# Optimization experiments

Hardware: AMD Instinct MI355X
Metric: run time of the kernel (lower is better)

The kernel has to match this reference:

```python
import jax, jax.numpy as jnp
import numpy as np

DIM = 768
HEADS = 12
HEAD_DIM = DIM // HEADS
SCALE = HEAD_DIM ** -0.5
EPS = 1e-6


def setup_inputs() -> dict:
    key = jax.random.key(0)
    ks = jax.random.split(key, 10)
    B, Nq, Nk, C = 4, 4096, 4096, DIM
    std = C ** -0.5
    return {
        "x_q": jax.random.normal(ks[0], (B, Nq, C), jnp.float32),
        "x_kv": jax.random.normal(ks[1], (B, Nk, C), jnp.float32),
        "Wq": jax.random.normal(ks[2], (C, C), jnp.float32) * std,
        "bq": jnp.zeros((C,), jnp.float32),
        "Wk": jax.random.normal(ks[3], (C, C), jnp.float32) * std,
        "bk": jnp.zeros((C,), jnp.float32),
        "Wv": jax.random.normal(ks[4], (C, C), jnp.float32) * std,
        "bv": jnp.zeros((C,), jnp.float32),
        "Wp": jax.random.normal(ks[5], (C, C), jnp.float32) * std,
        "bp": jnp.zeros((C,), jnp.float32),
    }


def _phi(x):
    # ELU(alpha=1) + 1 positive feature map
    return jax.nn.elu(x) + 1.0


def reference(x_q, x_kv, Wq, bq, Wk, bk, Wv, bv, Wp, bp):
    B, Nq, C = x_q.shape
    Nk = x_kv.shape[1]
    h, d = HEADS, HEAD_DIM
    # projections (torch Linear: x @ W.T + b)
    q = x_q @ Wq.T + bq   # [B,Nq,C]
    k = x_kv @ Wk.T + bk  # [B,Nk,C]
    v = x_kv @ Wv.T + bv  # [B,Nk,C]
    # split heads -> [B,h,N,d]
    q = q.reshape(B, Nq, h, d).transpose(0, 2, 1, 3) * SCALE
    k = k.reshape(B, Nk, h, d).transpose(0, 2, 1, 3)
    v = v.reshape(B, Nk, h, d).transpose(0, 2, 1, 3)
    q_phi = _phi(q)
    k_phi = _phi(k)
    # KV state [B,h,d,d] and normalizer sum [B,h,d]
    kv = jnp.einsum('bhnd,bhne->bhde', k_phi, v)
    k_sum = k_phi.sum(axis=2)
    out = jnp.einsum('bhnd,bhde->bhne', q_phi, kv)
    z = jnp.einsum('bhnd,bhd->bhn', q_phi, k_sum)[..., None] + EPS
    out = out / z
    out = out.transpose(0, 2, 1, 3).reshape(B, Nq, C)
    return out @ Wp.T + bp
```

## Files before the change

### kernel.cpp

```cpp
#include <hip/hip_runtime.h>
#include <hip/hip_bf16.h>
#include <cstdint>
#include <cstddef>

#define HD_B   4
#define SEQ    4096
#define CDIM   768
#define HEADS  12
#define HDIM   64
#define MROWS  (HD_B * SEQ)
#define QSCALE 0.125f
#define EPSV   1e-6f

typedef __attribute__((ext_vector_type(8))) short  short8v;
typedef __attribute__((ext_vector_type(4))) float  f32x4;

__device__ __forceinline__ unsigned short f2b(float f) {
    unsigned int u = __float_as_uint(f);
    u += 0x7FFFu + ((u >> 16) & 1u);
    return (unsigned short)(u >> 16);
}
__device__ __forceinline__ float b2f(unsigned short b) {
    return __uint_as_float(((unsigned int)b) << 16);
}
__device__ __forceinline__ float phi_f(float x) {
    return x > 0.f ? x + 1.f : __expf(x);
}

#define GLOAD_LDS16(g, l)                                             \
    __builtin_amdgcn_global_load_lds(                                 \
        (__attribute__((address_space(1))) void*)(void*)(g),          \
        (__attribute__((address_space(3))) void*)(l), 16, 0, 0)

#define VMW12() asm volatile("s_waitcnt vmcnt(12)" ::: "memory")
#define VMW8()  asm volatile("s_waitcnt vmcnt(8)"  ::: "memory")
#define VMW4()  asm volatile("s_waitcnt vmcnt(4)"  ::: "memory")
#define VMW0()  asm volatile("s_waitcnt vmcnt(0)"  ::: "memory")
#define LGW()   asm volatile("s_waitcnt lgkmcnt(0)" ::: "memory")
#define SB()    do { __builtin_amdgcn_sched_barrier(0);               \
                     __builtin_amdgcn_s_barrier();                    \
                     __builtin_amdgcn_sched_barrier(0); } while (0)

__global__ void wcvt_all(const float* __restrict__ wq, const float* __restrict__ wk,
                         const float* __restrict__ wv, const float* __restrict__ wp,
                         unsigned short* __restrict__ dst) {
    const int y = blockIdx.y;
    const float* src = (y == 0) ? wq : (y == 1) ? wk : (y == 2) ? wv : wp;
    const int i = blockIdx.x * 256 + threadIdx.x;
    float4 v = reinterpret_cast<const float4*>(src)[i];
    ushort4 o;
    o.x = f2b(v.x); o.y = f2b(v.y); o.z = f2b(v.z); o.w = f2b(v.w);
    reinterpret_cast<ushort4*>(dst + (size_t)y * (CDIM * CDIM))[i] = o;
}

template <int KIND>
__global__ __launch_bounds__(256) void gemm_cnt(
    const float* __restrict__ Aq,
    const float* __restrict__ Akv,
    const unsigned short* __restrict__ Abf,
    const unsigned short* __restrict__ Wb,
    const float* __restrict__ b0, const float* __restrict__ b1,
    const float* __restrict__ b2,
    unsigned short* __restrict__ out_q, unsigned short* __restrict__ out_k,
    unsigned short* __restrict__ out_v, float* __restrict__ out_f)
{
    constexpr int K  = CDIM;
    constexpr int NC = (KIND == 0) ? 18 : 6;
    constexpr int T  = NC * 128;
    constexpr int NT = K / 64;

    __shared__ __align__(16) char smem[65536];

    const int tid  = threadIdx.x;
    const int lane = tid & 63;
    const int w    = tid >> 6;
    const int wr   = w >> 1, wc = w & 1;

    const int bid  = blockIdx.x;
    const int s    = (bid & 7) * (T >> 3) + (bid >> 3);
    const int colp = s % NC;
    const int rowp = s / NC;
    const int brow = rowp * 128;
    const int mode = (KIND == 0) ? (colp / 6) : 3;
    const int bcol = (KIND == 0) ? (colp % 6) * 128 : colp * 128;

    const float* A32          = (KIND == 0) ? (mode == 0 ? Aq : Akv) : nullptr;
    const unsigned short* Bp  = Wb + ((KIND == 0) ? (size_t)mode * (K * K) : 0);

    const int r8  = lane >> 3;
    const int c8e = ((lane & 7) ^ r8) << 3;
    const int ar  = lane >> 4;
    const int ac  = (lane & 15) << 2;
    const int fr  = lane & 15;
    const int hi4 = lane >> 4;

    f32x4 acc[4][4];
#pragma unroll
    for (int i = 0; i < 4; ++i)
#pragma unroll
        for (int j = 0; j < 4; ++j)
            acc[i][j] = (f32x4){0.f, 0.f, 0.f, 0.f};

    auto stageB = [&](int buf, int kt) {
        char* dst = smem + 32768 + buf * 16384;
#pragma unroll
        for (int g = 0; g < 4; ++g) {
            const unsigned short* src =
                Bp + (size_t)(bcol + w * 32 + g * 8 + r8) * K + kt * 64 + c8e;
            GLOAD_LDS16(src, dst + (w * 32 + g * 8) * 128);
        }
    };
    auto stageA16 = [&](int buf, int kt) {
        char* dst = smem + buf * 16384;
#pragma unroll
        for (int g = 0; g < 4; ++g) {
            const unsigned short* src =
                Abf + (size_t)(brow + w * 32 + g * 8 + r8) * K + kt * 64 + c8e;
            GLOAD_LDS16(src, dst + (w * 32 + g * 8) * 128);
        }
    };
    float4 fA[8];
    auto aload = [&](int kt) {
#pragma unroll
        for (int j = 0; j < 8; ++j)
            fA[j] = *(const float4*)(A32 + (size_t)(brow + w * 32 + j * 4 + ar) * K
                                     + kt * 64 + ac);
    };
    auto awrite = [&](int buf) {
        char* dst = smem + buf * 16384;
#pragma unroll
        for (int j = 0; j < 8; ++j) {
            const int row = w * 32 + j * 4 + ar;
            unsigned int p0, p1;
            asm("v_cvt_pk_bf16_f32 %0, %1, %2" : "=v"(p0) : "v"(fA[j].x), "v"(fA[j].y));
            asm("v_cvt_pk_bf16_f32 %0, %1, %2" : "=v"(p1) : "v"(fA[j].z), "v"(fA[j].w));
            uint2 pk; pk.x = p0; pk.y = p1;
            *(uint2*)(dst + row * 128 + ((ac << 1) ^ ((row & 7) << 4))) = pk;
        }
    };
    auto compute = [&](int buf) {
        const char* Ab = smem + buf * 16384;
        const char* Bb = smem + 32768 + buf * 16384;
        short8v a[4][2];
#pragma unroll
        for (int i = 0; i < 4; ++i) {
            const int row = wr * 64 + i * 16 + fr;
#pragma unroll
            for (int ks = 0; ks < 2; ++ks)
                a[i][ks] = *(const short8v*)(Ab + row * 128 +
                              ((((ks << 2) + hi4) ^ (row & 7)) << 4));
        }
#pragma unroll
        for (int j = 0; j < 4; ++j) {
            const int row = wc * 64 + j * 16 + fr;
            short8v bb0 = *(const short8v*)(Bb + row * 128 + ((hi4 ^ (row & 7)) << 4));
            short8v bb1 = *(const short8v*)(Bb + row * 128 + (((4 + hi4) ^ (row & 7)) << 4));
#pragma unroll
            for (int i = 0; i < 4; ++i) {
                acc[i][j] = __builtin_amdgcn_mfma_f32_16x16x32_bf16(a[i][0], bb0, acc[i][j], 0, 0, 0);
                acc[i][j] = __builtin_amdgcn_mfma_f32_16x16x32_bf16(a[i][1], bb1, acc[i][j], 0, 0, 0);
            }
        }
    };

    if (KIND == 0) {
        aload(0);
        stageB(0, 0);
        VMW4();
        awrite(0);
        aload(1);
        stageB(1, 1);
        LGW();
        SB();
        for (int t = 0; t < NT; ++t) {
            const int c = t & 1;
            if (t == NT - 1) { VMW0(); } else { VMW12(); }
            SB();
            compute(c);
            SB();
            if (t < NT - 1) {
                VMW4();
                awrite(c ^ 1);
                if (t < NT - 2) { aload(t + 2); stageB(c, t + 2); }
                LGW();
            }
        }
    } else {
        stageA16(0, 0); stageB(0, 0);
        stageA16(1, 1); stageB(1, 1);
        for (int t = 0; t < NT; ++t) {
            const int c = t & 1;
            if (t == NT - 1) { VMW0(); } else { VMW8(); }
            SB();
            compute(c);
            SB();
            if (t < NT - 2) { stageA16(c, t + 2); stageB(c, t + 2); }
        }
    }

    float* ep = (float*)(void*)smem + w * (16 * 68);
    const int rr = lane >> 2;
    const int cb = (lane & 3) * 4;
    const float* bptr = (KIND == 1) ? b0 : (mode == 0 ? b0 : (mode == 1 ? b1 : b2));
    unsigned short* o16 = (KIND == 0)
        ? (mode == 0 ? out_q : (mode == 1 ? out_k : out_v)) : nullptr;

    float4 bb[4];
#pragma unroll
    for (int q = 0; q < 4; ++q)
        bb[q] = *(const float4*)&bptr[bcol + wc * 64 + q * 16 + cb];

#pragma unroll
    for (int i = 0; i < 4; ++i) {
#pragma unroll
        for (int j = 0; j < 4; ++j)
#pragma unroll
            for (int r = 0; r < 4; ++r)
                ep[(hi4 * 4 + r) * 68 + j * 16 + fr] = acc[i][j][r];
#pragma unroll
        for (int q = 0; q < 4; ++q) {
            const int cc = q * 16 + cb;
            f32x4 v = *(const f32x4*)&ep[rr * 68 + cc];
            const int rg = brow + wr * 64 + i * 16 + rr;
            const int cg = bcol + wc * 64 + cc;
            const float4 bq = bb[q];
            if (KIND == 1) {
                float4 ov;
                ov.x = v[0] + bq.x; ov.y = v[1] + bq.y;
                ov.z = v[2] + bq.z; ov.w = v[3] + bq.w;
                *(float4*)(out_f + (size_t)rg * 768 + cg) = ov;
            } else {
                ushort4 ov;
                if (mode == 0) {
                    ov.x = f2b(phi_f((v[0] + bq.x) * QSCALE));
                    ov.y = f2b(phi_f((v[1] + bq.y) * QSCALE));
                    ov.z = f2b(phi_f((v[2] + bq.z) * QSCALE));
                    ov.w = f2b(phi_f((v[3] + bq.w) * QSCALE));
                } else if (mode == 1) {
                    ov.x = f2b(phi_f(v[0] + bq.x));
                    ov.y = f2b(phi_f(v[1] + bq.y));
                    ov.z = f2b(phi_f(v[2] + bq.z));
                    ov.w = f2b(phi_f(v[3] + bq.w));
                } else {
                    ov.x = f2b(v[0] + bq.x);
                    ov.y = f2b(v[1] + bq.y);
                    ov.z = f2b(v[2] + bq.z);
                    ov.w = f2b(v[3] + bq.w);
                }
                *(ushort4*)(o16 + (size_t)rg * 768 + cg) = ov;
            }
        }
    }
}

#define KVCH   128
#define KVITER 2
#define NCHUNK 16

__global__ __launch_bounds__(256) void kv_part(
    const unsigned short* __restrict__ kphi,
    const unsigned short* __restrict__ vmat,
    float* __restrict__ part)
{
    const int bh = blockIdx.y;
    const int b  = bh / HEADS, h = bh % HEADS;
    const int c  = blockIdx.x;
    __shared__ float Kl[KVCH][HDIM];
    __shared__ float Vl[KVCH][HDIM];
    const int t  = threadIdx.x;
    const int i  = t >> 2;
    const int jb = t & 3;

    float acc[16];
#pragma unroll
    for (int jj = 0; jj < 16; ++jj) acc[jj] = 0.f;
    float ksum = 0.f;

    for (int it = 0; it < KVITER; ++it) {
        const size_t rbase = (size_t)b * SEQ + (size_t)c * (KVCH * KVITER) + it * KVCH;
        __syncthreads();
        for (int l = 0; l < KVCH / 32; ++l) {
            int row = l * 32 + (t >> 3);
            int col = (t & 7) << 3;
            const size_t g = (rbase + row) * CDIM + h * HDIM + col;
            int4 kk = *(const int4*)(kphi + g);
            int4 vv = *(const int4*)(vmat + g);
            const unsigned short* kp = (const unsigned short*)&kk;
            const unsigned short* vp = (const unsigned short*)&vv;
#pragma unroll
            for (int q = 0; q < 8; ++q) {
                Kl[row][col + q] = b2f(kp[q]);
                Vl[row][col + q] = b2f(vp[q]);
            }
        }
        __syncthreads();
        for (int n = 0; n < KVCH; ++n) {
            float kf = Kl[n][i];
            const float4* vr = (const float4*)&Vl[n][jb * 16];
            float4 v0 = vr[0], v1 = vr[1], v2 = vr[2], v3 = vr[3];
            acc[0]  += kf * v0.x; acc[1]  += kf * v0.y; acc[2]  += kf * v0.z; acc[3]  += kf * v0.w;
            acc[4]  += kf * v1.x; acc[5]  += kf * v1.y; acc[6]  += kf * v1.z; acc[7]  += kf * v1.w;
            acc[8]  += kf * v2.x; acc[9]  += kf * v2.y; acc[10] += kf * v2.z; acc[11] += kf * v2.w;
            acc[12] += kf * v3.x; acc[13] += kf * v3.y; acc[14] += kf * v3.z; acc[15] += kf * v3.w;
            ksum += kf;
        }
    }
    float* op = part + ((size_t)c * 48 + bh) * 4160;
#pragma unroll
    for (int jj = 0; jj < 16; ++jj) op[i * 64 + jb * 16 + jj] = acc[jj];
    if (jb == 0) op[4096 + i] = ksum;
}

__global__ void kv_finalize(const float* __restrict__ part, float* __restrict__ kv) {
    int idx = blockIdx.x * 256 + threadIdx.x;
    if (idx >= 48 * 4160) return;
    float s = 0.f;
    for (int c = 0; c < NCHUNK; ++c) s += part[(size_t)c * 48 * 4160 + idx];
    kv[idx] = s;
}

__global__ __launch_bounds__(256) void attn_apply(
    const unsigned short* __restrict__ qphi,
    const float* __restrict__ kv,
    unsigned short* __restrict__ attn)
{
    const int h  = blockIdx.y;
    const int m0 = blockIdx.x * 64;
    const int b  = m0 >> 12;
    const int bh = b * HEADS + h;
    __shared__ float kvs[HDIM][HDIM];
    __shared__ float ksums[HDIM];
    __shared__ unsigned short ql[64][HDIM];
    const int t = threadIdx.x;
    const float* kvp = kv + (size_t)bh * 4160;
#pragma unroll
    for (int it = 0; it < 4; ++it) {
        int e = it * 1024 + t * 4;
        *(float4*)&kvs[e >> 6][e & 63] = *(const float4*)&kvp[e];
    }
    if (t < 64) ksums[t] = kvp[4096 + t];
#pragma unroll
    for (int it = 0; it < 2; ++it) {
        int row = it * 32 + (t >> 3);
        int col = (t & 7) << 3;
        *(int4*)&ql[row][col] =
            *(const int4*)(qphi + (size_t)(m0 + row) * CDIM + h * HDIM + col);
    }
    __syncthreads();

    const int r  = t >> 2;
    const int jb = t & 3;
    float acc[16];
#pragma unroll
    for (int jj = 0; jj < 16; ++jj) acc[jj] = 0.f;
    float z = 0.f;
    for (int q8 = 0; q8 < 8; ++q8) {
        short8v qv = *(const short8v*)&ql[r][q8 * 8];
#pragma unroll
        for (int dd = 0; dd < 8; ++dd) {
            float qd = b2f((unsigned short)qv[dd]);
            int d = q8 * 8 + dd;
            const float4* kr = (const float4*)&kvs[d][jb * 16];
            float4 k0 = kr[0], k1 = kr[1], k2 = kr[2], k3 = kr[3];
            acc[0]  += qd * k0.x; acc[1]  += qd * k0.y; acc[2]  += qd * k0.z; acc[3]  += qd * k0.w;
            acc[4]  += qd * k1.x; acc[5]  += qd * k1.y; acc[6]  += qd * k1.z; acc[7]  += qd * k1.w;
            acc[8]  += qd * k2.x; acc[9]  += qd * k2.y; acc[10] += qd * k2.z; acc[11] += qd * k2.w;
            acc[12] += qd * k3.x; acc[13] += qd * k3.y; acc[14] += qd * k3.z; acc[15] += qd * k3.w;
            z += qd * ksums[d];
        }
    }
    const float inv = 1.f / (z + EPSV);
    unsigned short* op = attn + (size_t)(m0 + r) * CDIM + h * HDIM + jb * 16;
#pragma unroll
    for (int jj = 0; jj < 16; ++jj) op[jj] = f2b(acc[jj] * inv);
}

extern "C" void kernel_launch(void* const* d_in, const int* in_sizes, int n_in,
                              void* d_out, int out_size, void* d_ws, size_t ws_size,
                              hipStream_t stream)
{
    const float* x_q  = (const float*)d_in[0];
    const float* x_kv = (const float*)d_in[1];
    const float* Wq   = (const float*)d_in[2];
    const float* bq   = (const float*)d_in[3];
    const float* Wk   = (const float*)d_in[4];
    const float* bk   = (const float*)d_in[5];
    const float* Wv   = (const float*)d_in[6];
    const float* bv   = (const float*)d_in[7];
    const float* Wp   = (const float*)d_in[8];
    const float* bp   = (const float*)d_in[9];
    float* out = (float*)d_out;

    char* ws = (char*)d_ws;
    size_t off = 0;
    auto alloc = [&](size_t bytes) -> char* {
        char* p = ws + off;
        off += (bytes + 255) & ~(size_t)255;
        return p;
    };
    const size_t xelems = (size_t)MROWS * CDIM;
    const size_t welems = (size_t)CDIM * CDIM;

    unsigned short* w16    = (unsigned short*)alloc(4 * welems * 2);
    unsigned short* wp16   = w16 + 3 * welems;
    unsigned short* qphi   = (unsigned short*)alloc(xelems * 2);
    unsigned short* kphi   = (unsigned short*)alloc(xelems * 2);
    unsigned short* v16    = (unsigned short*)alloc(xelems * 2);
    unsigned short* attn16 = (unsigned short*)alloc(xelems * 2);
    float* part = (float*)alloc((size_t)NCHUNK * 48 * 4160 * 4);
    float* kvf  = (float*)alloc((size_t)48 * 4160 * 4);

    wcvt_all<<<dim3(576, 4), 256, 0, stream>>>(Wq, Wk, Wv, Wp, w16);

    gemm_cnt<0><<<2304, 256, 0, stream>>>(
        x_q, x_kv, nullptr, w16, bq, bk, bv, qphi, kphi, v16, nullptr);

    kv_part<<<dim3(NCHUNK, 48), 256, 0, stream>>>(kphi, v16, part);
    kv_finalize<<<(48 * 4160 + 255) / 256, 256, 0, stream>>>(part, kvf);
    attn_apply<<<dim3(MROWS / 64, HEADS), 256, 0, stream>>>(qphi, kvf, attn16);

    gemm_cnt<1><<<768, 256, 0, stream>>>(
        nullptr, nullptr, attn16, wp16, bp, nullptr, nullptr,
        nullptr, nullptr, nullptr, out);
}
```

Before: 223.0 us.

## Split Q projection into simple GEMM and single-buffer A tiles in KV/proj GEMMs

Replaces the fused QKV GEMM with a standalone single-buffered Q-projection kernel and a combined K/V GEMM that treats Wk and Wv as one contiguous 1536-row weight. The K/V and output-projection GEMMs now keep only a single LDS buffer for A (register-staged) with a double-buffered B, cutting shared memory from 64KB to 48KB and adding launch_bounds(256,3) to raise occupancy. The output-projection A tile moves from direct global-to-LDS loads to register staging. The cost is less latency hiding in the unpipelined Q kernel and an extra kernel launch.

```diff
diff --git a/kernel.cpp b/kernel.cpp
--- a/kernel.cpp
+++ b/kernel.cpp
@@ -53,39 +53,23 @@
     reinterpret_cast<ushort4*>(dst + (size_t)y * (CDIM * CDIM))[i] = o;
 }
 
-template <int KIND>
-__global__ __launch_bounds__(256) void gemm_cnt(
-    const float* __restrict__ Aq,
-    const float* __restrict__ Akv,
-    const unsigned short* __restrict__ Abf,
-    const unsigned short* __restrict__ Wb,
-    const float* __restrict__ b0, const float* __restrict__ b1,
-    const float* __restrict__ b2,
-    unsigned short* __restrict__ out_q, unsigned short* __restrict__ out_k,
-    unsigned short* __restrict__ out_v, float* __restrict__ out_f)
+__global__ __launch_bounds__(256) void gemm_q(
+    const float* __restrict__ A32,
+    const unsigned short* __restrict__ Bp,
+    const float* __restrict__ bias,
+    unsigned short* __restrict__ outp)
 {
-    constexpr int K  = CDIM;
-    constexpr int NC = (KIND == 0) ? 18 : 6;
-    constexpr int T  = NC * 128;
-    constexpr int NT = K / 64;
-
-    __shared__ __align__(16) char smem[65536];
+    constexpr int K = CDIM;
+    __shared__ __align__(16) char smem[32768];
+    char* As = smem;
+    char* Bs = smem + 16384;
 
     const int tid  = threadIdx.x;
     const int lane = tid & 63;
     const int w    = tid >> 6;
     const int wr   = w >> 1, wc = w & 1;
-
-    const int bid  = blockIdx.x;
-    const int s    = (bid & 7) * (T >> 3) + (bid >> 3);
-    const int colp = s % NC;
-    const int rowp = s / NC;
-    const int brow = rowp * 128;
-    const int mode = (KIND == 0) ? (colp / 6) : 3;
-    const int bcol = (KIND == 0) ? (colp % 6) * 128 : colp * 128;
-
-    const float* A32          = (KIND == 0) ? (mode == 0 ? Aq : Akv) : nullptr;
-    const unsigned short* Bp  = Wb + ((KIND == 0) ? (size_t)mode * (K * K) : 0);
+    const int brow = blockIdx.x * 128;
+    const int bcol = blockIdx.y * 128;
 
     const int r8  = lane >> 3;
     const int c8e = ((lane & 7) ^ r8) << 3;
@@ -101,115 +85,59 @@
         for (int j = 0; j < 4; ++j)
             acc[i][j] = (f32x4){0.f, 0.f, 0.f, 0.f};
 
-    auto stageB = [&](int buf, int kt) {
-        char* dst = smem + 32768 + buf * 16384;
+    for (int k0 = 0; k0 < K; k0 += 64) {
 #pragma unroll
         for (int g = 0; g < 4; ++g) {
             const unsigned short* src =
-                Bp + (size_t)(bcol + w * 32 + g * 8 + r8) * K + kt * 64 + c8e;
-            GLOAD_LDS16(src, dst + (w * 32 + g * 8) * 128);
-        }
-    };
-    auto stageA16 = [&](int buf, int kt) {
-        char* dst = smem + buf * 16384;
-#pragma unroll
-        for (int g = 0; g < 4; ++g) {
-            const unsigned short* src =
-                Abf + (size_t)(brow + w * 32 + g * 8 + r8) * K + kt * 64 + c8e;
-            GLOAD_LDS16(src, dst + (w * 32 + g * 8) * 128);
-        }
-    };
-    float4 fA[8];
-    auto aload = [&](int kt) {
-#pragma unroll
-        for (int j = 0; j < 8; ++j)
-            fA[j] = *(const float4*)(A32 + (size_t)(brow + w * 32 + j * 4 + ar) * K
-                                     + kt * 64 + ac);
-    };
-    auto awrite = [&](int buf) {
-        char* dst = smem + buf * 16384;
+                Bp + (size_t)(bcol + w * 32 + g * 8 + r8) * K + k0 + c8e;
+            GLOAD_LDS16(src, Bs + (w * 32 + g * 8) * 128);
+        }
 #pragma unroll
         for (int j = 0; j < 8; ++j) {
             const int row = w * 32 + j * 4 + ar;
+            float4 f = *(const float4*)(A32 + (size_t)(brow + row) * K + k0 + ac);
             unsigned int p0, p1;
-            asm("v_cvt_pk_bf16_f32 %0, %1, %2" : "=v"(p0) : "v"(fA[j].x), "v"(fA[j].y));
-            asm("v_cvt_pk_bf16_f32 %0, %1, %2" : "=v"(p1) : "v"(fA[j].z), "v"(fA[j].w));
+            asm("v_cvt_pk_bf16_f32 %0, %1, %2" : "=v"(p0) : "v"(f.x), "v"(f.y));
+            asm("v_cvt_pk_bf16_f32 %0, %1, %2" : "=v"(p1) : "v"(f.z), "v"(f.w));
             uint2 pk; pk.x = p0; pk.y = p1;
-            *(uint2*)(dst + row * 128 + ((ac << 1) ^ ((row & 7) << 4))) = pk;
-        }
-    };
-    auto compute = [&](int buf) {
-        const char* Ab = smem + buf * 16384;
-        const char* Bb = smem + 32768 + buf * 16384;
-        short8v a[4][2];
+            *(uint2*)(As + row * 128 + ((ac << 1) ^ ((row & 7) << 4))) = pk;
+        }
+        __syncthreads();
+
+        short8v a[4][2], b[4][2];
 #pragma unroll
         for (int i = 0; i < 4; ++i) {
             const int row = wr * 64 + i * 16 + fr;
 #pragma unroll
             for (int ks = 0; ks < 2; ++ks)
-                a[i][ks] = *(const short8v*)(Ab + row * 128 +
+                a[i][ks] = *(const short8v*)(As + row * 128 +
                               ((((ks << 2) + hi4) ^ (row & 7)) << 4));
         }
 #pragma unroll
         for (int j = 0; j < 4; ++j) {
             const int row = wc * 64 + j * 16 + fr;
-            short8v bb0 = *(const short8v*)(Bb + row * 128 + ((hi4 ^ (row & 7)) << 4));
-            short8v bb1 = *(const short8v*)(Bb + row * 128 + (((4 + hi4) ^ (row & 7)) << 4));
-#pragma unroll
-            for (int i = 0; i < 4; ++i) {
-                acc[i][j] = __builtin_amdgcn_mfma_f32_16x16x32_bf16(a[i][0], bb0, acc[i][j], 0, 0, 0);
-                acc[i][j] = __builtin_amdgcn_mfma_f32_16x16x32_bf16(a[i][1], bb1, acc[i][j], 0, 0, 0);
+#pragma unroll
+            for (int ks = 0; ks < 2; ++ks)
+                b[j][ks] = *(const short8v*)(Bs + row * 128 +
+                              ((((ks << 2) + hi4) ^ (row & 7)) << 4));
+        }
+#pragma unroll
+        for (int i = 0; i < 4; ++i)
+#pragma unroll
+            for (int j = 0; j < 4; ++j) {
+                acc[i][j] = __builtin_amdgcn_mfma_f32_16x16x32_bf16(a[i][0], b[j][0], acc[i][j], 0, 0, 0);
+                acc[i][j] = __builtin_amdgcn_mfma_f32_16x16x32_bf16(a[i][1], b[j][1], acc[i][j], 0, 0, 0);
             }
-        }
-    };
-
-    if (KIND == 0) {
-        aload(0);
-        stageB(0, 0);
-        VMW4();
-        awrite(0);
-        aload(1);
-        stageB(1, 1);
-        LGW();
-        SB();
-        for (int t = 0; t < NT; ++t) {
-            const int c = t & 1;
-            if (t == NT - 1) { VMW0(); } else { VMW12(); }
-            SB();
-            compute(c);
-            SB();
-            if (t < NT - 1) {
-                VMW4();
-                awrite(c ^ 1);
-                if (t < NT - 2) { aload(t + 2); stageB(c, t + 2); }
-                LGW();
-            }
-        }
-    } else {
-        stageA16(0, 0); stageB(0, 0);
-        stageA16(1, 1); stageB(1, 1);
-        for (int t = 0; t < NT; ++t) {
-            const int c = t & 1;
-            if (t == NT - 1) { VMW0(); } else { VMW8(); }
-            SB();
-            compute(c);
-            SB();
-            if (t < NT - 2) { stageA16(c, t + 2); stageB(c, t + 2); }
-        }
+        __syncthreads();
     }
 
     float* ep = (float*)(void*)smem + w * (16 * 68);
     const int rr = lane >> 2;
     const int cb = (lane & 3) * 4;
-    const float* bptr = (KIND == 1) ? b0 : (mode == 0 ? b0 : (mode == 1 ? b1 : b2));
-    unsigned short* o16 = (KIND == 0)
-        ? (mode == 0 ? out_q : (mode == 1 ? out_k : out_v)) : nullptr;
-
     float4 bb[4];
 #pragma unroll
     for (int q = 0; q < 4; ++q)
-        bb[q] = *(const float4*)&bptr[bcol + wc * 64 + q * 16 + cb];
-
+        bb[q] = *(const float4*)&bias[bcol + wc * 64 + q * 16 + cb];
 #pragma unroll
     for (int i = 0; i < 4; ++i) {
 #pragma unroll
@@ -224,19 +152,188 @@
             const int rg = brow + wr * 64 + i * 16 + rr;
             const int cg = bcol + wc * 64 + cc;
             const float4 bq = bb[q];
+            ushort4 ov;
+            ov.x = f2b(phi_f((v[0] + bq.x) * QSCALE));
+            ov.y = f2b(phi_f((v[1] + bq.y) * QSCALE));
+            ov.z = f2b(phi_f((v[2] + bq.z) * QSCALE));
+            ov.w = f2b(phi_f((v[3] + bq.w) * QSCALE));
+            *(ushort4*)(outp + (size_t)rg * 768 + cg) = ov;
+        }
+    }
+}
+
+template <int KIND>
+__global__ __launch_bounds__(256, 3) void gemm_p2(
+    const float* __restrict__ A32,
+    const unsigned short* __restrict__ Abf,
+    const unsigned short* __restrict__ Bp,
+    const float* __restrict__ b0, const float* __restrict__ b1,
+    unsigned short* __restrict__ out_k, unsigned short* __restrict__ out_v,
+    float* __restrict__ out_f)
+{
+    constexpr int K  = CDIM;
+    constexpr int NC = (KIND == 0) ? 12 : 6;
+    constexpr int T  = NC * 128;
+    constexpr int NT = K / 64;
+
+    __shared__ __align__(16) char smem[49152];
+    char* As = smem;
+
+    const int tid  = threadIdx.x;
+    const int lane = tid & 63;
+    const int w    = tid >> 6;
+    const int wr   = w >> 1, wc = w & 1;
+
+    const int bid  = blockIdx.x;
+    const int s    = (bid & 7) * (T >> 3) + (bid >> 3);
+    const int colp = s % NC;
+    const int rowp = s / NC;
+    const int brow = rowp * 128;
+    const int bcol = colp * 128;
+
+    const int r8  = lane >> 3;
+    const int c8e = ((lane & 7) ^ r8) << 3;
+    const int ar  = lane >> 4;
+    const int ac  = (lane & 15) << 2;
+    const int fr  = lane & 15;
+    const int hi4 = lane >> 4;
+
+    f32x4 acc[4][4];
+#pragma unroll
+    for (int i = 0; i < 4; ++i)
+#pragma unroll
+        for (int j = 0; j < 4; ++j)
+            acc[i][j] = (f32x4){0.f, 0.f, 0.f, 0.f};
+
+    auto stageB = [&](int buf, int kt) {
+        char* dst = smem + 16384 + buf * 16384;
+#pragma unroll
+        for (int g = 0; g < 4; ++g) {
+            const unsigned short* src =
+                Bp + (size_t)(bcol + w * 32 + g * 8 + r8) * K + kt * 64 + c8e;
+            GLOAD_LDS16(src, dst + (w * 32 + g * 8) * 128);
+        }
+    };
+
+    float4 fA[8];
+    int4   rAb[4];
+    auto aload = [&](int kt) {
+        if (KIND == 0) {
+#pragma unroll
+            for (int j = 0; j < 8; ++j)
+                fA[j] = *(const float4*)(A32 + (size_t)(brow + w * 32 + j * 4 + ar) * K
+                                         + kt * 64 + ac);
+        } else {
+#pragma unroll
+            for (int g = 0; g < 4; ++g)
+                rAb[g] = *(const int4*)(Abf + (size_t)(brow + w * 32 + g * 8 + r8) * K
+                                        + kt * 64 + ((lane & 7) << 3));
+        }
+    };
+    auto awrite = [&]() {
+        if (KIND == 0) {
+#pragma unroll
+            for (int j = 0; j < 8; ++j) {
+                const int row = w * 32 + j * 4 + ar;
+                unsigned int p0, p1;
+                asm("v_cvt_pk_bf16_f32 %0, %1, %2" : "=v"(p0) : "v"(fA[j].x), "v"(fA[j].y));
+                asm("v_cvt_pk_bf16_f32 %0, %1, %2" : "=v"(p1) : "v"(fA[j].z), "v"(fA[j].w));
+                uint2 pk; pk.x = p0; pk.y = p1;
+                *(uint2*)(As + row * 128 + ((ac << 1) ^ ((row & 7) << 4))) = pk;
+            }
+        } else {
+#pragma unroll
+            for (int g = 0; g < 4; ++g) {
+                const int row = w * 32 + g * 8 + r8;
+                *(int4*)(As + row * 128 + (((lane & 7) ^ r8) << 4)) = rAb[g];
+            }
+        }
+    };
+    auto compute = [&](int bbuf) {
+        const char* Bb = smem + 16384 + bbuf * 16384;
+        short8v a[4][2];
+#pragma unroll
+        for (int i = 0; i < 4; ++i) {
+            const int row = wr * 64 + i * 16 + fr;
+#pragma unroll
+            for (int ks = 0; ks < 2; ++ks)
+                a[i][ks] = *(const short8v*)(As + row * 128 +
+                              ((((ks << 2) + hi4) ^ (row & 7)) << 4));
+        }
+#pragma unroll
+        for (int j = 0; j < 4; ++j) {
+            const int row = wc * 64 + j * 16 + fr;
+            short8v bb0 = *(const short8v*)(Bb + row * 128 + ((hi4 ^ (row & 7)) << 4));
+            short8v bb1 = *(const short8v*)(Bb + row * 128 + (((4 + hi4) ^ (row & 7)) << 4));
+#pragma unroll
+            for (int i = 0; i < 4; ++i) {
+                acc[i][j] = __builtin_amdgcn_mfma_f32_16x16x32_bf16(a[i][0], bb0, acc[i][j], 0, 0, 0);
+                acc[i][j] = __builtin_amdgcn_mfma_f32_16x16x32_bf16(a[i][1], bb1, acc[i][j], 0, 0, 0);
+            }
+        }
+    };
+
+    aload(0);
+    stageB(0, 0);
+    VMW4();
+    awrite();
+    aload(1);
+    stageB(1, 1);
+    LGW();
+    SB();
+
+    for (int t = 0; t < NT; ++t) {
+        const int c = t & 1;
+        if (t == NT - 1) { VMW0(); }
+        else if (KIND == 0) { VMW12(); }
+        else { VMW8(); }
+        SB();
+        compute(c);
+        SB();
+        if (t < NT - 1) {
+            VMW4();
+            awrite();
+            if (t < NT - 2) { aload(t + 2); stageB(c, t + 2); }
+            LGW();
+        }
+    }
+
+    float* ep = (float*)(void*)smem + w * (16 * 68);
+    const int rr = lane >> 2;
+    const int cb = (lane & 3) * 4;
+    const bool isV = (KIND == 0) && (colp >= 6);
+    const float* bptr = (KIND == 1) ? b0 : (isV ? (b1 + (bcol - 768)) : (b0 + bcol));
+    const int colbase = ((KIND == 0 && isV) ? bcol - 768 : bcol) + wc * 64;
+    unsigned short* o16 = isV ? out_v : out_k;
+
+    float4 bb[4];
+#pragma unroll
+    for (int q = 0; q < 4; ++q)
+        bb[q] = (KIND == 1)
+            ? *(const float4*)&bptr[bcol + wc * 64 + q * 16 + cb]
+            : *(const float4*)&bptr[wc * 64 + q * 16 + cb];
+
+#pragma unroll
+    for (int i = 0; i < 4; ++i) {
+#pragma unroll
+        for (int j = 0; j < 4; ++j)
+#pragma unroll
+            for (int r = 0; r < 4; ++r)
+                ep[(hi4 * 4 + r) * 68 + j * 16 + fr] = acc[i][j][r];
+#pragma unroll
+        for (int q = 0; q < 4; ++q) {
+            const int cc = q * 16 + cb;
+            f32x4 v = *(const f32x4*)&ep[rr * 68 + cc];
+            const int rg = brow + wr * 64 + i * 16 + rr;
+            const float4 bq = bb[q];
             if (KIND == 1) {
                 float4 ov;
                 ov.x = v[0] + bq.x; ov.y = v[1] + bq.y;
                 ov.z = v[2] + bq.z; ov.w = v[3] + bq.w;
-                *(float4*)(out_f + (size_t)rg * 768 + cg) = ov;
+                *(float4*)(out_f + (size_t)rg * 768 + (bcol + wc * 64 + cc)) = ov;
             } else {
                 ushort4 ov;
-                if (mode == 0) {
-                    ov.x = f2b(phi_f((v[0] + bq.x) * QSCALE));
-                    ov.y = f2b(phi_f((v[1] + bq.y) * QSCALE));
-                    ov.z = f2b(phi_f((v[2] + bq.z) * QSCALE));
-                    ov.w = f2b(phi_f((v[3] + bq.w) * QSCALE));
-                } else if (mode == 1) {
+                if (!isV) {
                     ov.x = f2b(phi_f(v[0] + bq.x));
                     ov.y = f2b(phi_f(v[1] + bq.y));
                     ov.z = f2b(phi_f(v[2] + bq.z));
@@ -247,7 +344,7 @@
                     ov.z = f2b(v[2] + bq.z);
                     ov.w = f2b(v[3] + bq.w);
                 }
-                *(ushort4*)(o16 + (size_t)rg * 768 + cg) = ov;
+                *(ushort4*)(o16 + (size_t)rg * 768 + (colbase + cc)) = ov;
             }
         }
     }
@@ -402,6 +499,7 @@
     const size_t welems = (size_t)CDIM * CDIM;
 
     unsigned short* w16    = (unsigned short*)alloc(4 * welems * 2);
+    unsigned short* wkv16  = w16 + welems;
     unsigned short* wp16   = w16 + 3 * welems;
     unsigned short* qphi   = (unsigned short*)alloc(xelems * 2);
     unsigned short* kphi   = (unsigned short*)alloc(xelems * 2);
@@ -412,14 +510,15 @@
 
     wcvt_all<<<dim3(576, 4), 256, 0, stream>>>(Wq, Wk, Wv, Wp, w16);
 
-    gemm_cnt<0><<<2304, 256, 0, stream>>>(
-        x_q, x_kv, nullptr, w16, bq, bk, bv, qphi, kphi, v16, nullptr);
+    gemm_q<<<dim3(128, 6), 256, 0, stream>>>(x_q, w16, bq, qphi);
+
+    gemm_p2<0><<<1536, 256, 0, stream>>>(
+        x_kv, nullptr, wkv16, bk, bv, kphi, v16, nullptr);
 
     kv_part<<<dim3(NCHUNK, 48), 256, 0, stream>>>(kphi, v16, part);
     kv_finalize<<<(48 * 4160 + 255) / 256, 256, 0, stream>>>(part, kvf);
     attn_apply<<<dim3(MROWS / 64, HEADS), 256, 0, stream>>>(qphi, kvf, attn16);
 
-    gemm_cnt<1><<<768, 256, 0, stream>>>(
-        nullptr, nullptr, attn16, wp16, bp, nullptr, nullptr,
-        nullptr, nullptr, nullptr, out);
-}
+    gemm_p2<1><<<768, 256, 0, stream>>>(
+        nullptr, attn16, wp16, bp, nullptr, nullptr, nullptr, out);
+}
```

Result: slower. 242.2 us (+8.6%).

## Enlarge projection GEMM tiles to 256x128 with 512-thread blocks

Applied to the files above, without the earlier changes.

Both projection GEMMs now use 256x128 output tiles computed by 8 waves instead of 128x128 tiles computed by 4 waves. This halves how often each weight tile is re-read per output row. The A operand is staged through registers into a single LDS buffer, which also changes the output GEMM from direct global-to-LDS loads to register prefetch. B stays double-buffered, and the vmcnt wait thresholds are retuned to match. This gives fewer blocks and more per-block LDS and register pressure, and the single A buffer may reduce how much load latency is overlapped with compute.

```diff
diff --git a/kernel.cpp b/kernel.cpp
--- a/kernel.cpp
+++ b/kernel.cpp
@@ -32,9 +32,9 @@
         (__attribute__((address_space(1))) void*)(void*)(g),          \
         (__attribute__((address_space(3))) void*)(l), 16, 0, 0)
 
-#define VMW12() asm volatile("s_waitcnt vmcnt(12)" ::: "memory")
-#define VMW8()  asm volatile("s_waitcnt vmcnt(8)"  ::: "memory")
-#define VMW4()  asm volatile("s_waitcnt vmcnt(4)"  ::: "memory")
+#define VMW10() asm volatile("s_waitcnt vmcnt(10)" ::: "memory")
+#define VMW6()  asm volatile("s_waitcnt vmcnt(6)"  ::: "memory")
+#define VMW2()  asm volatile("s_waitcnt vmcnt(2)"  ::: "memory")
 #define VMW0()  asm volatile("s_waitcnt vmcnt(0)"  ::: "memory")
 #define LGW()   asm volatile("s_waitcnt lgkmcnt(0)" ::: "memory")
 #define SB()    do { __builtin_amdgcn_sched_barrier(0);               \
@@ -54,9 +54,8 @@
 }
 
 template <int KIND>
-__global__ __launch_bounds__(256) void gemm_cnt(
-    const float* __restrict__ Aq,
-    const float* __restrict__ Akv,
+__device__ __forceinline__ void gemm_body(
+    const float* __restrict__ Aq32, const float* __restrict__ Akv32,
     const unsigned short* __restrict__ Abf,
     const unsigned short* __restrict__ Wb,
     const float* __restrict__ b0, const float* __restrict__ b1,
@@ -66,26 +65,28 @@
 {
     constexpr int K  = CDIM;
     constexpr int NC = (KIND == 0) ? 18 : 6;
-    constexpr int T  = NC * 128;
+    constexpr int T  = NC * 64;
     constexpr int NT = K / 64;
 
     __shared__ __align__(16) char smem[65536];
+    char* As = smem;
 
     const int tid  = threadIdx.x;
     const int lane = tid & 63;
     const int w    = tid >> 6;
-    const int wr   = w >> 1, wc = w & 1;
+    const int wrow = w >> 1;
+    const int wcol = w & 1;
 
     const int bid  = blockIdx.x;
     const int s    = (bid & 7) * (T >> 3) + (bid >> 3);
     const int colp = s % NC;
     const int rowp = s / NC;
-    const int brow = rowp * 128;
+    const int brow = rowp * 256;
     const int mode = (KIND == 0) ? (colp / 6) : 3;
-    const int bcol = (KIND == 0) ? (colp % 6) * 128 : colp * 128;
-
-    const float* A32          = (KIND == 0) ? (mode == 0 ? Aq : Akv) : nullptr;
-    const unsigned short* Bp  = Wb + ((KIND == 0) ? (size_t)mode * (K * K) : 0);
+    const int bcolRel = (KIND == 0) ? (colp % 6) * 128 : colp * 128;
+
+    const float* A32 = (KIND == 0) ? (mode == 0 ? Aq32 : Akv32) : nullptr;
+    const unsigned short* Bp = Wb + ((KIND == 0) ? (size_t)mode * (K * K) : 0);
 
     const int r8  = lane >> 3;
     const int c8e = ((lane & 7) ^ r8) << 3;
@@ -104,55 +105,61 @@
     auto stageB = [&](int buf, int kt) {
         char* dst = smem + 32768 + buf * 16384;
 #pragma unroll
-        for (int g = 0; g < 4; ++g) {
+        for (int g = 0; g < 2; ++g) {
             const unsigned short* src =
-                Bp + (size_t)(bcol + w * 32 + g * 8 + r8) * K + kt * 64 + c8e;
-            GLOAD_LDS16(src, dst + (w * 32 + g * 8) * 128);
+                Bp + (size_t)(bcolRel + w * 16 + g * 8 + r8) * K + kt * 64 + c8e;
+            GLOAD_LDS16(src, dst + (w * 16 + g * 8) * 128);
         }
     };
-    auto stageA16 = [&](int buf, int kt) {
-        char* dst = smem + buf * 16384;
-#pragma unroll
-        for (int g = 0; g < 4; ++g) {
-            const unsigned short* src =
-                Abf + (size_t)(brow + w * 32 + g * 8 + r8) * K + kt * 64 + c8e;
-            GLOAD_LDS16(src, dst + (w * 32 + g * 8) * 128);
+
+    float4 fA[8];
+    int4   rAb[4];
+    auto aload = [&](int kt) {
+        if (KIND == 0) {
+#pragma unroll
+            for (int j = 0; j < 8; ++j)
+                fA[j] = *(const float4*)(A32 + (size_t)(brow + w * 32 + j * 4 + ar) * K
+                                         + kt * 64 + ac);
+        } else {
+#pragma unroll
+            for (int g = 0; g < 4; ++g)
+                rAb[g] = *(const int4*)(Abf + (size_t)(brow + w * 32 + g * 8 + r8) * K
+                                        + kt * 64 + ((lane & 7) << 3));
         }
     };
-    float4 fA[8];
-    auto aload = [&](int kt) {
-#pragma unroll
-        for (int j = 0; j < 8; ++j)
-            fA[j] = *(const float4*)(A32 + (size_t)(brow + w * 32 + j * 4 + ar) * K
-                                     + kt * 64 + ac);
+    auto awrite = [&]() {
+        if (KIND == 0) {
+#pragma unroll
+            for (int j = 0; j < 8; ++j) {
+                const int row = w * 32 + j * 4 + ar;
+                unsigned int p0, p1;
+                asm("v_cvt_pk_bf16_f32 %0, %1, %2" : "=v"(p0) : "v"(fA[j].x), "v"(fA[j].y));
+                asm("v_cvt_pk_bf16_f32 %0, %1, %2" : "=v"(p1) : "v"(fA[j].z), "v"(fA[j].w));
+                uint2 pk; pk.x = p0; pk.y = p1;
+                *(uint2*)(As + row * 128 + ((ac << 1) ^ ((row & 7) << 4))) = pk;
+            }
+        } else {
+#pragma unroll
+            for (int g = 0; g < 4; ++g) {
+                const int row = w * 32 + g * 8 + r8;
+                *(int4*)(As + row * 128 + (((lane & 7) ^ r8) << 4)) = rAb[g];
+            }
+        }
     };
-    auto awrite = [&](int buf) {
-        char* dst = smem + buf * 16384;
-#pragma unroll
-        for (int j = 0; j < 8; ++j) {
-            const int row = w * 32 + j * 4 + ar;
-            unsigned int p0, p1;
-            asm("v_cvt_pk_bf16_f32 %0, %1, %2" : "=v"(p0) : "v"(fA[j].x), "v"(fA[j].y));
-            asm("v_cvt_pk_bf16_f32 %0, %1, %2" : "=v"(p1) : "v"(fA[j].z), "v"(fA[j].w));
-            uint2 pk; pk.x = p0; pk.y = p1;
-            *(uint2*)(dst + row * 128 + ((ac << 1) ^ ((row & 7) << 4))) = pk;
-        }
-    };
-    auto compute = [&](int buf) {
-        const char* Ab = smem + buf * 16384;
-        const char* Bb = smem + 32768 + buf * 16384;
+    auto compute = [&](int bbuf) {
+        const char* Bb = smem + 32768 + bbuf * 16384;
         short8v a[4][2];
 #pragma unroll
         for (int i = 0; i < 4; ++i) {
-            const int row = wr * 64 + i * 16 + fr;
+            const int row = wrow * 64 + i * 16 + fr;
 #pragma unroll
             for (int ks = 0; ks < 2; ++ks)
-                a[i][ks] = *(const short8v*)(Ab + row * 128 +
+                a[i][ks] = *(const short8v*)(As + row * 128 +
                               ((((ks << 2) + hi4) ^ (row & 7)) << 4));
         }
 #pragma unroll
         for (int j = 0; j < 4; ++j) {
-            const int row = wc * 64 + j * 16 + fr;
+            const int row = wcol * 64 + j * 16 + fr;
             short8v bb0 = *(const short8v*)(Bb + row * 128 + ((hi4 ^ (row & 7)) << 4));
             short8v bb1 = *(const short8v*)(Bb + row * 128 + (((4 + hi4) ^ (row & 7)) << 4));
 #pragma unroll
@@ -163,52 +170,43 @@
         }
     };
 
-    if (KIND == 0) {
-        aload(0);
-        stageB(0, 0);
-        VMW4();
-        awrite(0);
-        aload(1);
-        stageB(1, 1);
-        LGW();
+    aload(0);
+    stageB(0, 0);
+    VMW2();
+    awrite();
+    aload(1);
+    stageB(1, 1);
+    LGW();
+    SB();
+
+    for (int t = 0; t < NT; ++t) {
+        const int c = t & 1;
+        if (t == NT - 1) { VMW0(); }
+        else if (KIND == 0) { VMW10(); }
+        else { VMW6(); }
         SB();
-        for (int t = 0; t < NT; ++t) {
-            const int c = t & 1;
-            if (t == NT - 1) { VMW0(); } else { VMW12(); }
-            SB();
-            compute(c);
-            SB();
-            if (t < NT - 1) {
-                VMW4();
-                awrite(c ^ 1);
-                if (t < NT - 2) { aload(t + 2); stageB(c, t + 2); }
-                LGW();
-            }
-        }
-    } else {
-        stageA16(0, 0); stageB(0, 0);
-        stageA16(1, 1); stageB(1, 1);
-        for (int t = 0; t < NT; ++t) {
-            const int c = t & 1;
-            if (t == NT - 1) { VMW0(); } else { VMW8(); }
-            SB();
-            compute(c);
-            SB();
-            if (t < NT - 2) { stageA16(c, t + 2); stageB(c, t + 2); }
+        compute(c);
+        SB();
+        if (t < NT - 1) {
+            VMW2();
+            awrite();
+            if (t < NT - 2) { aload(t + 2); stageB(c, t + 2); }
+            LGW();
         }
     }
 
     float* ep = (float*)(void*)smem + w * (16 * 68);
     const int rr = lane >> 2;
     const int cb = (lane & 3) * 4;
-    const float* bptr = (KIND == 1) ? b0 : (mode == 0 ? b0 : (mode == 1 ? b1 : b2));
+    const float* bptr = (KIND == 1) ? (b0 + bcolRel)
+                       : (mode == 0 ? (b0 + bcolRel) : (mode == 1 ? (b1 + bcolRel) : (b2 + bcolRel)));
     unsigned short* o16 = (KIND == 0)
         ? (mode == 0 ? out_q : (mode == 1 ? out_k : out_v)) : nullptr;
 
     float4 bb[4];
 #pragma unroll
     for (int q = 0; q < 4; ++q)
-        bb[q] = *(const float4*)&bptr[bcol + wc * 64 + q * 16 + cb];
+        bb[q] = *(const float4*)&bptr[wcol * 64 + q * 16 + cb];
 
 #pragma unroll
     for (int i = 0; i < 4; ++i) {
@@ -221,8 +219,8 @@
         for (int q = 0; q < 4; ++q) {
             const int cc = q * 16 + cb;
             f32x4 v = *(const f32x4*)&ep[rr * 68 + cc];
-            const int rg = brow + wr * 64 + i * 16 + rr;
-            const int cg = bcol + wc * 64 + cc;
+            const int rg = brow + wrow * 64 + i * 16 + rr;
+            const int cg = bcolRel + wcol * 64 + cc;
             const float4 bq = bb[q];
             if (KIND == 1) {
                 float4 ov;
@@ -253,6 +251,26 @@
     }
 }
 
+__global__ __launch_bounds__(512, 2) void gemm_qkv(
+    const float* __restrict__ xq, const float* __restrict__ xkv,
+    const unsigned short* __restrict__ w16,
+    const float* __restrict__ bq, const float* __restrict__ bk,
+    const float* __restrict__ bv,
+    unsigned short* __restrict__ qo, unsigned short* __restrict__ ko,
+    unsigned short* __restrict__ vo)
+{
+    gemm_body<0>(xq, xkv, nullptr, w16, bq, bk, bv, qo, ko, vo, nullptr);
+}
+
+__global__ __launch_bounds__(512, 2) void gemm_out(
+    const unsigned short* __restrict__ a16,
+    const unsigned short* __restrict__ wp,
+    const float* __restrict__ bp, float* __restrict__ outp)
+{
+    gemm_body<1>(nullptr, nullptr, a16, wp, bp, nullptr, nullptr,
+                 nullptr, nullptr, nullptr, outp);
+}
+
 #define KVCH   128
 #define KVITER 2
 #define NCHUNK 16
@@ -412,14 +430,11 @@
 
     wcvt_all<<<dim3(576, 4), 256, 0, stream>>>(Wq, Wk, Wv, Wp, w16);
 
-    gemm_cnt<0><<<2304, 256, 0, stream>>>(
-        x_q, x_kv, nullptr, w16, bq, bk, bv, qphi, kphi, v16, nullptr);
+    gemm_qkv<<<1152, 512, 0, stream>>>(x_q, x_kv, w16, bq, bk, bv, qphi, kphi, v16);
 
     kv_part<<<dim3(NCHUNK, 48), 256, 0, stream>>>(kphi, v16, part);
     kv_finalize<<<(48 * 4160 + 255) / 256, 256, 0, stream>>>(part, kvf);
     attn_apply<<<dim3(MROWS / 64, HEADS), 256, 0, stream>>>(qphi, kvf, attn16);
 
-    gemm_cnt<1><<<768, 256, 0, stream>>>(
-        nullptr, nullptr, attn16, wp16, bp, nullptr, nullptr,
-        nullptr, nullptr, nullptr, out);
-}
+    gemm_out<<<384, 512, 0, stream>>>(attn16, wp16, bp, out);
+}
```

Measured after the change: 280.2 us. 25.7% more time.
